# Kernel tuning notes

Measured on AMD Instinct MI355X. Metric: run time of the kernel, lower is better.

Reference implementation:

```python
import jax, jax.numpy as jnp
import numpy as np

NP_, B_ = 44, 400000

def setup_inputs() -> dict:
    key = jax.random.key(0)
    k_x, k1, k2, k3, k4 = jax.random.split(key, 5)
    return {
        "X": jax.random.normal(k_x, (NP_, 1, B_), dtype=jnp.float32),
        "lin1s": jax.random.normal(k1, (NP_, 4, 1), dtype=jnp.float32),
        "lin2s": jax.random.normal(k2, (NP_, 8, 4), dtype=jnp.float32),
        "lin3s": jax.random.normal(k3, (NP_, 4, 8), dtype=jnp.float32),
        "lin4s": jax.random.normal(k4, (NP_, 1, 4), dtype=jnp.float32),
    }

def reference(X, lin1s, lin2s, lin3s, lin4s):
    # forward_all: chained batched tiny GEMMs with ReLU, 'lik,lkj->lij'
    h = jax.nn.relu(jnp.einsum('lik,lkj->lij', lin1s, X))   # (NP, 4, B)
    h = jax.nn.relu(jnp.einsum('lik,lkj->lij', lin2s, h))   # (NP, 8, B)
    h = jax.nn.relu(jnp.einsum('lik,lkj->lij', lin3s, h))   # (NP, 4, B)
    return jnp.einsum('lik,lkj->lij', lin4s, h)             # (NP, 1, B)
```

## Files before the change

### kernel.cpp

```cpp
#include <hip/hip_runtime.h>

#define NP    44
#define B     400000
#define B4    (B / 4)
#define BLK   256
#define CPT   8
#define CHUNK (BLK * CPT)

typedef float f4 __attribute__((ext_vector_type(4)));

__device__ __forceinline__ void collapse_weights(
    const float* __restrict__ p1, const float* __restrict__ p2,
    const float* __restrict__ p3, const float* __restrict__ p4,
    float& gp, float& gn)
{
    float w1p[4], w1n[4];
#pragma unroll
    for (int k = 0; k < 4; ++k) {
        float w = p1[k];
        w1p[k] = fmaxf(w, 0.0f);
        w1n[k] = fminf(w, 0.0f);
    }

    float d2p[8], d2n[8];
#pragma unroll
    for (int i = 0; i < 8; ++i) {
        float ap = 0.0f, an = 0.0f;
#pragma unroll
        for (int k = 0; k < 4; ++k) {
            float w = p2[i * 4 + k];
            ap = fmaf(w, w1p[k], ap);
            an = fmaf(w, w1n[k], an);
        }
        d2p[i] = fmaxf(ap, 0.0f);
        d2n[i] = fminf(an, 0.0f);
    }

    float f3p[4], f3n[4];
#pragma unroll
    for (int j = 0; j < 4; ++j) {
        float ap = 0.0f, an = 0.0f;
#pragma unroll
        for (int i = 0; i < 8; ++i) {
            float w = p3[j * 8 + i];
            ap = fmaf(w, d2p[i], ap);
            an = fmaf(w, d2n[i], an);
        }
        f3p[j] = fmaxf(ap, 0.0f);
        f3n[j] = fminf(an, 0.0f);
    }

    gp = 0.0f; gn = 0.0f;
#pragma unroll
    for (int j = 0; j < 4; ++j) {
        gp = fmaf(p4[j], f3p[j], gp);
        gn = fmaf(p4[j], f3n[j], gn);
    }
}

__device__ __forceinline__ f4 apply_gain(f4 v, float gp, float gn)
{
    f4 r;
    r.x = v.x * (v.x >= 0.0f ? gp : gn);
    r.y = v.y * (v.y >= 0.0f ? gp : gn);
    r.z = v.z * (v.z >= 0.0f ? gp : gn);
    r.w = v.w * (v.w >= 0.0f ? gp : gn);
    return r;
}

__global__ __launch_bounds__(BLK) void collapsed_mlp_kernel(
    const float* __restrict__ X,
    const float* __restrict__ W1,
    const float* __restrict__ W2,
    const float* __restrict__ W3,
    const float* __restrict__ W4,
    float* __restrict__ out)
{
    const int l    = blockIdx.y;
    const int base = blockIdx.x * CHUNK + threadIdx.x;

    const f4* Xp = (const f4*)(X + (size_t)l * B);
    f4*       Op = (f4*)(out + (size_t)l * B);

    const bool full = (blockIdx.x + 1) * CHUNK <= B4;

    f4 xv[CPT];
    if (full) {
#pragma unroll
        for (int c = 0; c < CPT; ++c) xv[c] = Xp[base + c * BLK];
    }

    float gp, gn;
    collapse_weights(W1 + l * 4, W2 + l * 32, W3 + l * 32, W4 + l * 4, gp, gn);

    if (full) {
#pragma unroll
        for (int c = 0; c < CPT; ++c) {
            __builtin_nontemporal_store(apply_gain(xv[c], gp, gn),
                                        &Op[base + c * BLK]);
        }
    } else {
#pragma unroll
        for (int c = 0; c < CPT; ++c) {
            const int idx = base + c * BLK;
            if (idx < B4) {
                f4 v = Xp[idx];
                __builtin_nontemporal_store(apply_gain(v, gp, gn), &Op[idx]);
            }
        }
    }
}

extern "C" void kernel_launch(void* const* d_in, const int* in_sizes, int n_in,
                              void* d_out, int out_size, void* d_ws, size_t ws_size,
                              hipStream_t stream) {
    const float* X  = (const float*)d_in[0];
    const float* W1 = (const float*)d_in[1];
    const float* W2 = (const float*)d_in[2];
    const float* W3 = (const float*)d_in[3];
    const float* W4 = (const float*)d_in[4];
    float* out = (float*)d_out;

    dim3 grid((B4 + CHUNK - 1) / CHUNK, NP);
    collapsed_mlp_kernel<<<grid, BLK, 0, stream>>>(X, W1, W2, W3, W4, out);
}
```

Before: 127.2 us.

## Flatten work into exactly 2048 balanced blocks spanning layer boundaries

```diff
diff --git a/kernel.cpp b/kernel.cpp
--- a/kernel.cpp
+++ b/kernel.cpp
@@ -4,8 +4,10 @@
 #define B     400000
 #define B4    (B / 4)
 #define BLK   256
-#define CPT   8
-#define CHUNK (BLK * CPT)
+#define NBLK  2048
+#define TOT   (NP * B4)
+#define QW    (TOT / NBLK)
+#define RW    (TOT % NBLK)
 
 typedef float f4 __attribute__((ext_vector_type(4)));
 
@@ -76,38 +78,49 @@
     const float* __restrict__ W4,
     float* __restrict__ out)
 {
-    const int l    = blockIdx.y;
-    const int base = blockIdx.x * CHUNK + threadIdx.x;
+    const int b     = blockIdx.x;
+    const int tid   = threadIdx.x;
+    const int start = b * QW + min(b, RW);
+    const int count = QW + (b < RW ? 1 : 0);
 
-    const f4* Xp = (const f4*)(X + (size_t)l * B);
-    f4*       Op = (f4*)(out + (size_t)l * B);
+    const f4* Xp = (const f4*)X;
+    f4*       Op = (f4*)out;
 
-    const bool full = (blockIdx.x + 1) * CHUNK <= B4;
+    f4 xv[8];
+#pragma unroll
+    for (int c = 0; c < 8; ++c)
+        xv[c] = __builtin_nontemporal_load(&Xp[start + tid + c * BLK]);
 
-    f4 xv[CPT];
-    if (full) {
-#pragma unroll
-        for (int c = 0; c < CPT; ++c) xv[c] = Xp[base + c * BLK];
+    const int  extra = count - 8 * BLK;
+    const bool has9  = tid < extra;
+    f4 x9;
+    if (has9)
+        x9 = __builtin_nontemporal_load(&Xp[start + tid + 8 * BLK]);
+
+    const int l0    = start / B4;
+    const int l1    = (start + count - 1) / B4;
+    const int bound = (l0 + 1) * B4;
+
+    float g0p, g0n, g1p, g1n;
+    collapse_weights(W1 + l0 * 4, W2 + l0 * 32, W3 + l0 * 32, W4 + l0 * 4, g0p, g0n);
+    if (l1 != l0) {
+        collapse_weights(W1 + l1 * 4, W2 + l1 * 32, W3 + l1 * 32, W4 + l1 * 4, g1p, g1n);
+    } else {
+        g1p = g0p; g1n = g0n;
     }
 
-    float gp, gn;
-    collapse_weights(W1 + l * 4, W2 + l * 32, W3 + l * 32, W4 + l * 4, gp, gn);
-
-    if (full) {
 #pragma unroll
-        for (int c = 0; c < CPT; ++c) {
-            __builtin_nontemporal_store(apply_gain(xv[c], gp, gn),
-                                        &Op[base + c * BLK]);
-        }
-    } else {
-#pragma unroll
-        for (int c = 0; c < CPT; ++c) {
-            const int idx = base + c * BLK;
-            if (idx < B4) {
-                f4 v = Xp[idx];
-                __builtin_nontemporal_store(apply_gain(v, gp, gn), &Op[idx]);
-            }
-        }
+    for (int c = 0; c < 8; ++c) {
+        const int   idx = start + tid + c * BLK;
+        const float gp  = (idx >= bound) ? g1p : g0p;
+        const float gn  = (idx >= bound) ? g1n : g0n;
+        __builtin_nontemporal_store(apply_gain(xv[c], gp, gn), &Op[idx]);
+    }
+    if (has9) {
+        const int   idx = start + tid + 8 * BLK;
+        const float gp  = (idx >= bound) ? g1p : g0p;
+        const float gn  = (idx >= bound) ? g1n : g0n;
+        __builtin_nontemporal_store(apply_gain(x9, gp, gn), &Op[idx]);
     }
 }
 
@@ -121,6 +134,5 @@
     const float* W4 = (const float*)d_in[4];
     float* out = (float*)d_out;
 
-    dim3 grid((B4 + CHUNK - 1) / CHUNK, NP);
-    collapsed_mlp_kernel<<<grid, BLK, 0, stream>>>(X, W1, W2, W3, W4, out);
+    collapsed_mlp_kernel<<<dim3(NBLK), BLK, 0, stream>>>(X, W1, W2, W3, W4, out);
 }
```

New measurement: 129.4 us. About the same (+1.7%).
